# Optimization experiments

Hardware: AMD Instinct MI355X
Metric: run time of the kernel (lower is better)

## Reference

```python
import jax, jax.numpy as jnp
import numpy as np

NUM_HEADS = 16

def setup_inputs() -> dict:
    key = jax.random.key(0)
    k1, k2, k3, k4 = jax.random.split(key, 4)
    B, S, E = 4, 2048, 1024
    return {
        "q": jax.random.normal(k1, (B, S, E), dtype=jnp.float32),
        "k": jax.random.normal(k2, (B, S, E), dtype=jnp.float32),
        "v": jax.random.normal(k3, (B, S, E), dtype=jnp.float32),
        "w_out": jax.random.normal(k4, (E, E), dtype=jnp.float32) * (E ** -0.5),
        "b_out": jnp.zeros((E,), dtype=jnp.float32),
    }

def reference(q, k, v, w_out, b_out):
    B, S, E = q.shape
    H = NUM_HEADS
    D = E // H
    scale = D ** -0.5
    # split heads: [B, S, E] -> [B, H, S, D]
    def split(x):
        return x.reshape(B, S, H, D).transpose(0, 2, 1, 3)
    qh, kh, vh = split(q), split(k), split(v)
    scores = jnp.einsum('bhqd,bhkd->bhqk', qh, kh) * scale  # [B,H,S,S]
    weights = jax.nn.softmax(scores, axis=-1)
    # dropout is identity in eval mode
    out = jnp.einsum('bhqk,bhkd->bhqd', weights, vh)
    out = out.transpose(0, 2, 1, 3).reshape(B, S, E)  # merge heads
    return out @ w_out.T + b_out
```

## Files before the change

kernel.cpp:

```cpp
#include <hip/hip_runtime.h>
#include <cstdint>
#include <cstddef>

typedef __attribute__((ext_vector_type(8))) short bf16x8;
typedef __attribute__((ext_vector_type(4))) float f32x4;
typedef __attribute__((ext_vector_type(16))) float f32x16;

#define MFMA16(a, b, c) __builtin_amdgcn_mfma_f32_16x16x32_bf16((a), (b), (c), 0, 0, 0)
#define MFMA32(a, b, c) __builtin_amdgcn_mfma_f32_32x32x16_bf16((a), (b), (c), 0, 0, 0)

constexpr int Bz = 4, S = 2048, E = 1024, H = 16, Dh = 64;
constexpr size_t BSE = (size_t)Bz * S * E;
constexpr int LDP = 72;
constexpr int VLD = 136;

__device__ __forceinline__ unsigned short f2bf(float f) {
    uint32_t u = __builtin_bit_cast(uint32_t, f);
    u += 0x7FFFu + ((u >> 16) & 1u);
    return (unsigned short)(u >> 16);
}

__device__ __forceinline__ float exp2_fast(float x) {
#if __has_builtin(__builtin_amdgcn_exp2f)
    return __builtin_amdgcn_exp2f(x);
#else
    return exp2f(x);
#endif
}

__device__ __forceinline__ uint32_t pack_bf16(float a, float b) {
    uint32_t ua = __builtin_bit_cast(uint32_t, a) + 0x8000u;
    uint32_t ub = __builtin_bit_cast(uint32_t, b) + 0x8000u;
#if __has_builtin(__builtin_amdgcn_perm)
    return __builtin_amdgcn_perm(ub, ua, 0x07060302u);
#else
    return (ua >> 16) | (ub & 0xFFFF0000u);
#endif
}

__global__ __launch_bounds__(256) void convert_kernel(const float* __restrict__ in,
                                                      unsigned short* __restrict__ out,
                                                      int n4, float scale) {
    int i = blockIdx.x * blockDim.x + threadIdx.x;
    if (i < n4) {
        float4 f = ((const float4*)in)[i];
        ushort4 u;
        u.x = f2bf(f.x * scale);
        u.y = f2bf(f.y * scale);
        u.z = f2bf(f.z * scale);
        u.w = f2bf(f.w * scale);
        ((ushort4*)out)[i] = u;
    }
}

__global__ __launch_bounds__(256) void transpose_v_kernel(const float* __restrict__ v,
                                                          unsigned short* __restrict__ vt) {
    __shared__ unsigned short tile[64][65];
    const int b = blockIdx.z, h = blockIdx.y, s0 = blockIdx.x * 64;
    const int r = threadIdx.x >> 2, cb = (threadIdx.x & 3) * 16;

    const float* src = v + ((size_t)(b * S + s0 + r) * E + h * Dh + cb);
#pragma unroll
    for (int j = 0; j < 16; j += 4) {
        float4 f = *(const float4*)(src + j);
        tile[cb + j + 0][r] = f2bf(f.x);
        tile[cb + j + 1][r] = f2bf(f.y);
        tile[cb + j + 2][r] = f2bf(f.z);
        tile[cb + j + 3][r] = f2bf(f.w);
    }
    __syncthreads();
    const int dv = threadIdx.x >> 2, seg = (threadIdx.x & 3) * 16;
    unsigned short* dst = vt + (((size_t)(b * H + h) * Dh + dv) * S + s0 + seg);
    uint4 w0, w1;
    const unsigned short* trow = &tile[dv][seg];
    w0 = *(const uint4*)(trow);
    w1 = *(const uint4*)(trow + 8);
    *(uint4*)(dst) = w0;
    *(uint4*)(dst + 8) = w1;
}

__global__ __launch_bounds__(256, 4) void attn_kernel(const float* __restrict__ q,
                                                      const unsigned short* __restrict__ kb,
                                                      const unsigned short* __restrict__ vt,
                                                      unsigned short* __restrict__ attn) {
    __shared__ unsigned short smem[128 * LDP + 64 * VLD];
    unsigned short* Ks = smem;
    unsigned short* Vts = smem + 128 * LDP;

    const int b = blockIdx.z, h = blockIdx.y, qblk = blockIdx.x;
    const int tid = threadIdx.x;
    const int wave = tid >> 6, lane = tid & 63;
    const int l32 = lane & 31, half = lane >> 5;

    const int q0 = qblk * 128 + wave * 32;
    const float scl = 0.125f * 1.44269504088896f;

    bf16x8 qreg[4];
    {
        const float* qsrc = q + ((size_t)(b * S + q0 + l32)) * E + h * Dh + half * 8;
#pragma unroll
        for (int t = 0; t < 4; ++t) {
            float4 f0 = *(const float4*)(qsrc + 16 * t);
            float4 f1 = *(const float4*)(qsrc + 16 * t + 4);
            bf16x8 r;
            r[0] = (short)f2bf(f0.x * scl); r[1] = (short)f2bf(f0.y * scl);
            r[2] = (short)f2bf(f0.z * scl); r[3] = (short)f2bf(f0.w * scl);
            r[4] = (short)f2bf(f1.x * scl); r[5] = (short)f2bf(f1.y * scl);
            r[6] = (short)f2bf(f1.z * scl); r[7] = (short)f2bf(f1.w * scl);
            qreg[t] = r;
        }
    }

    f32x16 oacc[2];
#pragma unroll
    for (int mt = 0; mt < 2; ++mt)
#pragma unroll
        for (int r = 0; r < 16; ++r) oacc[mt][r] = 0.f;
    float lp0 = 0.f, lp1 = 0.f, lp2 = 0.f, lp3 = 0.f;

    const int krow = tid >> 1, kseg = (tid & 1) * 32;
    const int vrow = tid >> 2, vseg = (tid & 3) * 32;
    const unsigned short* kbase = kb + ((size_t)(b * S) * E + h * Dh);
    const unsigned short* vbase = vt + ((size_t)((b * H + h) * Dh + vrow) * S);

    for (int kt = 0; kt < S / 128; ++kt) {
        __syncthreads();
        {
            const uint4* ksrc = (const uint4*)(kbase + (size_t)(kt * 128 + krow) * E + kseg);
            uint4* kdst = (uint4*)(Ks + krow * LDP + kseg);
#pragma unroll
            for (int u = 0; u < 4; ++u) kdst[u] = ksrc[u];
            const uint4* vsrc = (const uint4*)(vbase + kt * 128 + vseg);
            uint4* vdst = (uint4*)(Vts + vrow * VLD + vseg);
#pragma unroll
            for (int u = 0; u < 4; ++u) vdst[u] = vsrc[u];
        }
        __syncthreads();

#pragma unroll
        for (int kh = 0; kh < 2; ++kh) {
            f32x16 st[2];
#pragma unroll
            for (int mt = 0; mt < 2; ++mt) {
#pragma unroll
                for (int r = 0; r < 16; ++r) st[mt][r] = 0.f;
#pragma unroll
                for (int t = 0; t < 4; ++t) {
                    bf16x8 a = *(const bf16x8*)(Ks + (kh * 64 + mt * 32 + l32) * LDP +
                                                t * 16 + half * 8);
                    st[mt] = MFMA32(a, qreg[t], st[mt]);
                }
            }

            uint32_t pkd[2][4][2];
#pragma unroll
            for (int mt = 0; mt < 2; ++mt)
#pragma unroll
                for (int g = 0; g < 4; ++g) {
                    float p0 = exp2_fast(st[mt][4 * g + 0]);
                    float p1 = exp2_fast(st[mt][4 * g + 1]);
                    float p2 = exp2_fast(st[mt][4 * g + 2]);
                    float p3 = exp2_fast(st[mt][4 * g + 3]);
                    lp0 += p0; lp1 += p1; lp2 += p2; lp3 += p3;
                    pkd[mt][g][0] = pack_bf16(p0, p1);
                    pkd[mt][g][1] = pack_bf16(p2, p3);
                }

#pragma unroll
            for (int c = 0; c < 4; ++c) {
                const int ms = c >> 1;
                const int g0 = 2 * (c & 1);
                uint32_t a0 = pkd[ms][g0][0], a1 = pkd[ms][g0][1];
                uint32_t b0 = pkd[ms][g0 + 1][0], b1 = pkd[ms][g0 + 1][1];
                uint32_t snd0 = half ? a0 : b0;
                uint32_t snd1 = half ? a1 : b1;
                uint32_t r0 = (uint32_t)__shfl_xor((int)snd0, 32);
                uint32_t r1 = (uint32_t)__shfl_xor((int)snd1, 32);
                int4 bi;
                bi.x = (int)(half ? r0 : a0);
                bi.y = (int)(half ? r1 : a1);
                bi.z = (int)(half ? b0 : r0);
                bi.w = (int)(half ? b1 : r1);
                bf16x8 bfrag = __builtin_bit_cast(bf16x8, bi);
#pragma unroll
                for (int mt = 0; mt < 2; ++mt) {
                    bf16x8 a = *(const bf16x8*)(Vts + (mt * 32 + l32) * VLD +
                                                kh * 64 + c * 16 + half * 8);
                    oacc[mt] = MFMA32(a, bfrag, oacc[mt]);
                }
            }
        }
    }

    __syncthreads();
    float l_part = (lp0 + lp1) + (lp2 + lp3);
    float l = l_part + (float)__shfl_xor(l_part, 32);
    float inv = 1.0f / l;

    unsigned short* ob = smem + wave * (32 * LDP);
#pragma unroll
    for (int mt = 0; mt < 2; ++mt)
#pragma unroll
        for (int g = 0; g < 4; ++g) {
            int dv0 = 8 * g + 4 * half + 32 * mt;
            uint2 w2;
            w2.x = pack_bf16(oacc[mt][4 * g + 0] * inv, oacc[mt][4 * g + 1] * inv);
            w2.y = pack_bf16(oacc[mt][4 * g + 2] * inv, oacc[mt][4 * g + 3] * inv);
            *(uint2*)(ob + l32 * LDP + dv0) = w2;
        }
    __syncthreads();
    {
        int row = lane >> 1;
        int cg0 = (lane & 1) * 4;
        unsigned short* gdst = attn + ((size_t)(b * S + q0 + row)) * E + h * Dh;
#pragma unroll
        for (int j = 0; j < 4; ++j) {
            bf16x8 v8 = *(const bf16x8*)(ob + row * LDP + (cg0 + j) * 8);
            *(bf16x8*)(gdst + (cg0 + j) * 8) = v8;
        }
    }
}

constexpr int PLD = 40;
__global__ __launch_bounds__(256) void proj_kernel(const unsigned short* __restrict__ A,
                                                   const unsigned short* __restrict__ W,
                                                   const float* __restrict__ bias,
                                                   float* __restrict__ C) {
    __shared__ unsigned short As[128 * PLD];
    __shared__ unsigned short Bs[128 * PLD];
    const int tid = threadIdx.x;
    const int wave = tid >> 6, lane = tid & 63, quad = lane >> 4, l16 = lane & 15;
    const int wm = wave >> 1, wn = wave & 1;
    const int m0 = blockIdx.x * 128, n0 = blockIdx.y * 128;

    f32x4 acc[4][4];
    f32x4 zero = {0.f, 0.f, 0.f, 0.f};
#pragma unroll
    for (int mi = 0; mi < 4; ++mi)
#pragma unroll
        for (int ni = 0; ni < 4; ++ni) acc[mi][ni] = zero;

    const int srow = tid >> 1, scb = (tid & 1) * 16;

    for (int k0 = 0; k0 < 1024; k0 += 32) {
        __syncthreads();
        {
            const uint4* asrc = (const uint4*)(A + (size_t)(m0 + srow) * 1024 + k0 + scb);
            uint4* adst = (uint4*)(As + srow * PLD + scb);
            adst[0] = asrc[0];
            adst[1] = asrc[1];
            const uint4* bsrc = (const uint4*)(W + (size_t)(n0 + srow) * 1024 + k0 + scb);
            uint4* bdst = (uint4*)(Bs + srow * PLD + scb);
            bdst[0] = bsrc[0];
            bdst[1] = bsrc[1];
        }
        __syncthreads();

        bf16x8 af[4], bfr[4];
#pragma unroll
        for (int mi = 0; mi < 4; ++mi)
            af[mi] = *(const bf16x8*)(As + (wm * 64 + mi * 16 + l16) * PLD + quad * 8);
#pragma unroll
        for (int ni = 0; ni < 4; ++ni)
            bfr[ni] = *(const bf16x8*)(Bs + (wn * 64 + ni * 16 + l16) * PLD + quad * 8);
#pragma unroll
        for (int mi = 0; mi < 4; ++mi)
#pragma unroll
            for (int ni = 0; ni < 4; ++ni)
                acc[mi][ni] = MFMA16(af[mi], bfr[ni], acc[mi][ni]);
    }

    float bb[4];
#pragma unroll
    for (int ni = 0; ni < 4; ++ni) bb[ni] = bias[n0 + wn * 64 + ni * 16 + l16];
#pragma unroll
    for (int mi = 0; mi < 4; ++mi) {
        const int row = m0 + wm * 64 + mi * 16 + quad * 4;
#pragma unroll
        for (int ni = 0; ni < 4; ++ni) {
            const int col = n0 + wn * 64 + ni * 16 + l16;
#pragma unroll
            for (int r = 0; r < 4; ++r)
                C[(size_t)(row + r) * 1024 + col] = acc[mi][ni][r] + bb[ni];
        }
    }
}

extern "C" void kernel_launch(void* const* d_in, const int* in_sizes, int n_in,
                              void* d_out, int out_size, void* d_ws, size_t ws_size,
                              hipStream_t stream) {
    const float* q = (const float*)d_in[0];
    const float* k = (const float*)d_in[1];
    const float* v = (const float*)d_in[2];
    const float* w = (const float*)d_in[3];
    const float* bias = (const float*)d_in[4];
    float* out = (float*)d_out;

    unsigned short* ws = (unsigned short*)d_ws;
    unsigned short* kb = ws;
    unsigned short* vt = kb + BSE;
    unsigned short* wb = vt + BSE;
    unsigned short* attnb = wb + (size_t)E * E;

    {
        int n4 = (int)(BSE / 4);
        convert_kernel<<<dim3((n4 + 255) / 256), dim3(256), 0, stream>>>(k, kb, n4, 1.0f);
        int nw4 = (int)((size_t)E * E / 4);
        convert_kernel<<<dim3((nw4 + 255) / 256), dim3(256), 0, stream>>>(w, wb, nw4, 1.0f);
    }
    transpose_v_kernel<<<dim3(S / 64, H, Bz), dim3(256), 0, stream>>>(v, vt);
    attn_kernel<<<dim3(S / 128, H, Bz), dim3(256), 0, stream>>>(q, kb, vt, attnb);
    proj_kernel<<<dim3((Bz * S) / 128, E / 128), dim3(256), 0, stream>>>(attnb, wb, bias, out);
}
```

Baseline: 287.9 us.

## Fuse K/V prep, prefetch tiles in registers, remap blocks, use 32x32 MFMA projection

```diff
diff --git a/kernel.cpp b/kernel.cpp
--- a/kernel.cpp
+++ b/kernel.cpp
@@ -6,7 +6,6 @@
 typedef __attribute__((ext_vector_type(4))) float f32x4;
 typedef __attribute__((ext_vector_type(16))) float f32x16;
 
-#define MFMA16(a, b, c) __builtin_amdgcn_mfma_f32_16x16x32_bf16((a), (b), (c), 0, 0, 0)
 #define MFMA32(a, b, c) __builtin_amdgcn_mfma_f32_32x32x16_bf16((a), (b), (c), 0, 0, 0)
 
 constexpr int Bz = 4, S = 2048, E = 1024, H = 16, Dh = 64;
@@ -38,45 +37,43 @@
 #endif
 }
 
-__global__ __launch_bounds__(256) void convert_kernel(const float* __restrict__ in,
-                                                      unsigned short* __restrict__ out,
-                                                      int n4, float scale) {
-    int i = blockIdx.x * blockDim.x + threadIdx.x;
-    if (i < n4) {
-        float4 f = ((const float4*)in)[i];
-        ushort4 u;
-        u.x = f2bf(f.x * scale);
-        u.y = f2bf(f.y * scale);
-        u.z = f2bf(f.z * scale);
-        u.w = f2bf(f.w * scale);
-        ((ushort4*)out)[i] = u;
-    }
-}
-
-__global__ __launch_bounds__(256) void transpose_v_kernel(const float* __restrict__ v,
-                                                          unsigned short* __restrict__ vt) {
+__global__ __launch_bounds__(256) void prep_kv(const float* __restrict__ k,
+                                               const float* __restrict__ v,
+                                               unsigned short* __restrict__ kb,
+                                               unsigned short* __restrict__ vt) {
     __shared__ unsigned short tile[64][65];
     const int b = blockIdx.z, h = blockIdx.y, s0 = blockIdx.x * 64;
     const int r = threadIdx.x >> 2, cb = (threadIdx.x & 3) * 16;
-
-    const float* src = v + ((size_t)(b * S + s0 + r) * E + h * Dh + cb);
-#pragma unroll
-    for (int j = 0; j < 16; j += 4) {
-        float4 f = *(const float4*)(src + j);
-        tile[cb + j + 0][r] = f2bf(f.x);
-        tile[cb + j + 1][r] = f2bf(f.y);
-        tile[cb + j + 2][r] = f2bf(f.z);
-        tile[cb + j + 3][r] = f2bf(f.w);
+    const size_t off = (size_t)(b * S + s0 + r) * E + h * Dh + cb;
+
+    {
+        const float* src = k + off;
+        uint32_t o[8];
+#pragma unroll
+        for (int j = 0; j < 8; ++j) {
+            float2 f = *(const float2*)(src + 2 * j);
+            o[j] = pack_bf16(f.x, f.y);
+        }
+        unsigned short* dst = kb + off;
+        *(uint4*)(dst) = *(const uint4*)(o);
+        *(uint4*)(dst + 8) = *(const uint4*)(o + 4);
+    }
+    {
+        const float* src = v + off;
+#pragma unroll
+        for (int j = 0; j < 16; j += 4) {
+            float4 f = *(const float4*)(src + j);
+            tile[cb + j + 0][r] = f2bf(f.x);
+            tile[cb + j + 1][r] = f2bf(f.y);
+            tile[cb + j + 2][r] = f2bf(f.z);
+            tile[cb + j + 3][r] = f2bf(f.w);
+        }
     }
     __syncthreads();
     const int dv = threadIdx.x >> 2, seg = (threadIdx.x & 3) * 16;
     unsigned short* dst = vt + (((size_t)(b * H + h) * Dh + dv) * S + s0 + seg);
-    uint4 w0, w1;
-    const unsigned short* trow = &tile[dv][seg];
-    w0 = *(const uint4*)(trow);
-    w1 = *(const uint4*)(trow + 8);
-    *(uint4*)(dst) = w0;
-    *(uint4*)(dst + 8) = w1;
+    *(uint4*)(dst) = *(const uint4*)(&tile[dv][seg]);
+    *(uint4*)(dst + 8) = *(const uint4*)(&tile[dv][seg] + 8);
 }
 
 __global__ __launch_bounds__(256, 4) void attn_kernel(const float* __restrict__ q,
@@ -87,7 +84,11 @@
     unsigned short* Ks = smem;
     unsigned short* Vts = smem + 128 * LDP;
 
-    const int b = blockIdx.z, h = blockIdx.y, qblk = blockIdx.x;
+    const int wid = blockIdx.x + 16 * (blockIdx.y + 16 * blockIdx.z);
+    const int c_ = wid & 7, j_ = wid >> 3;
+    const int bh = c_ * 8 + (j_ >> 4), qblk = j_ & 15;
+    const int b = bh >> 4, h = bh & 15;
+
     const int tid = threadIdx.x;
     const int wave = tid >> 6, lane = tid & 63;
     const int l32 = lane & 31, half = lane >> 5;
@@ -123,19 +124,36 @@
     const unsigned short* kbase = kb + ((size_t)(b * S) * E + h * Dh);
     const unsigned short* vbase = vt + ((size_t)((b * H + h) * Dh + vrow) * S);
 
+    uint4 kpre[4], vpre[4];
+    {
+        const uint4* ksrc = (const uint4*)(kbase + (size_t)krow * E + kseg);
+#pragma unroll
+        for (int u = 0; u < 4; ++u) kpre[u] = ksrc[u];
+        const uint4* vsrc = (const uint4*)(vbase + vseg);
+#pragma unroll
+        for (int u = 0; u < 4; ++u) vpre[u] = vsrc[u];
+    }
+
     for (int kt = 0; kt < S / 128; ++kt) {
         __syncthreads();
         {
-            const uint4* ksrc = (const uint4*)(kbase + (size_t)(kt * 128 + krow) * E + kseg);
             uint4* kdst = (uint4*)(Ks + krow * LDP + kseg);
 #pragma unroll
-            for (int u = 0; u < 4; ++u) kdst[u] = ksrc[u];
-            const uint4* vsrc = (const uint4*)(vbase + kt * 128 + vseg);
+            for (int u = 0; u < 4; ++u) kdst[u] = kpre[u];
             uint4* vdst = (uint4*)(Vts + vrow * VLD + vseg);
 #pragma unroll
-            for (int u = 0; u < 4; ++u) vdst[u] = vsrc[u];
+            for (int u = 0; u < 4; ++u) vdst[u] = vpre[u];
         }
         __syncthreads();
+
+        if (kt + 1 < S / 128) {
+            const uint4* ksrc = (const uint4*)(kbase + (size_t)((kt + 1) * 128 + krow) * E + kseg);
+#pragma unroll
+            for (int u = 0; u < 4; ++u) kpre[u] = ksrc[u];
+            const uint4* vsrc = (const uint4*)(vbase + (kt + 1) * 128 + vseg);
+#pragma unroll
+            for (int u = 0; u < 4; ++u) vpre[u] = vsrc[u];
+        }
 
 #pragma unroll
         for (int kh = 0; kh < 2; ++kh) {
@@ -222,66 +240,98 @@
 }
 
 constexpr int PLD = 40;
-__global__ __launch_bounds__(256) void proj_kernel(const unsigned short* __restrict__ A,
-                                                   const unsigned short* __restrict__ W,
-                                                   const float* __restrict__ bias,
-                                                   float* __restrict__ C) {
+__global__ __launch_bounds__(256, 4) void proj_kernel(const unsigned short* __restrict__ A,
+                                                      const float* __restrict__ W,
+                                                      const float* __restrict__ bias,
+                                                      float* __restrict__ C) {
     __shared__ unsigned short As[128 * PLD];
     __shared__ unsigned short Bs[128 * PLD];
     const int tid = threadIdx.x;
-    const int wave = tid >> 6, lane = tid & 63, quad = lane >> 4, l16 = lane & 15;
+    const int wave = tid >> 6, lane = tid & 63;
+    const int l32 = lane & 31, half = lane >> 5;
     const int wm = wave >> 1, wn = wave & 1;
     const int m0 = blockIdx.x * 128, n0 = blockIdx.y * 128;
 
-    f32x4 acc[4][4];
-    f32x4 zero = {0.f, 0.f, 0.f, 0.f};
-#pragma unroll
-    for (int mi = 0; mi < 4; ++mi)
-#pragma unroll
-        for (int ni = 0; ni < 4; ++ni) acc[mi][ni] = zero;
+    f32x16 acc[2][2];
+#pragma unroll
+    for (int mi = 0; mi < 2; ++mi)
+#pragma unroll
+        for (int ni = 0; ni < 2; ++ni)
+#pragma unroll
+            for (int r = 0; r < 16; ++r) acc[mi][ni][r] = 0.f;
 
     const int srow = tid >> 1, scb = (tid & 1) * 16;
+
+    uint4 apre[2];
+    float4 wpre[4];
+    {
+        const uint4* asrc = (const uint4*)(A + (size_t)(m0 + srow) * 1024 + scb);
+        apre[0] = asrc[0];
+        apre[1] = asrc[1];
+        const float4* wsrc = (const float4*)(W + (size_t)(n0 + srow) * 1024 + scb);
+#pragma unroll
+        for (int u = 0; u < 4; ++u) wpre[u] = wsrc[u];
+    }
 
     for (int k0 = 0; k0 < 1024; k0 += 32) {
         __syncthreads();
         {
-            const uint4* asrc = (const uint4*)(A + (size_t)(m0 + srow) * 1024 + k0 + scb);
             uint4* adst = (uint4*)(As + srow * PLD + scb);
-            adst[0] = asrc[0];
-            adst[1] = asrc[1];
-            const uint4* bsrc = (const uint4*)(W + (size_t)(n0 + srow) * 1024 + k0 + scb);
+            adst[0] = apre[0];
+            adst[1] = apre[1];
+            uint32_t pw[8];
+            const float* wf = (const float*)wpre;
+#pragma unroll
+            for (int j = 0; j < 8; ++j) pw[j] = pack_bf16(wf[2 * j], wf[2 * j + 1]);
             uint4* bdst = (uint4*)(Bs + srow * PLD + scb);
-            bdst[0] = bsrc[0];
-            bdst[1] = bsrc[1];
+            bdst[0] = *(const uint4*)(pw);
+            bdst[1] = *(const uint4*)(pw + 4);
         }
         __syncthreads();
 
-        bf16x8 af[4], bfr[4];
-#pragma unroll
-        for (int mi = 0; mi < 4; ++mi)
-            af[mi] = *(const bf16x8*)(As + (wm * 64 + mi * 16 + l16) * PLD + quad * 8);
-#pragma unroll
-        for (int ni = 0; ni < 4; ++ni)
-            bfr[ni] = *(const bf16x8*)(Bs + (wn * 64 + ni * 16 + l16) * PLD + quad * 8);
-#pragma unroll
-        for (int mi = 0; mi < 4; ++mi)
-#pragma unroll
-            for (int ni = 0; ni < 4; ++ni)
-                acc[mi][ni] = MFMA16(af[mi], bfr[ni], acc[mi][ni]);
-    }
-
-    float bb[4];
-#pragma unroll
-    for (int ni = 0; ni < 4; ++ni) bb[ni] = bias[n0 + wn * 64 + ni * 16 + l16];
-#pragma unroll
-    for (int mi = 0; mi < 4; ++mi) {
-        const int row = m0 + wm * 64 + mi * 16 + quad * 4;
-#pragma unroll
-        for (int ni = 0; ni < 4; ++ni) {
-            const int col = n0 + wn * 64 + ni * 16 + l16;
-#pragma unroll
-            for (int r = 0; r < 4; ++r)
-                C[(size_t)(row + r) * 1024 + col] = acc[mi][ni][r] + bb[ni];
+        if (k0 + 32 < 1024) {
+            const uint4* asrc = (const uint4*)(A + (size_t)(m0 + srow) * 1024 + k0 + 32 + scb);
+            apre[0] = asrc[0];
+            apre[1] = asrc[1];
+            const float4* wsrc = (const float4*)(W + (size_t)(n0 + srow) * 1024 + k0 + 32 + scb);
+#pragma unroll
+            for (int u = 0; u < 4; ++u) wpre[u] = wsrc[u];
+        }
+
+        bf16x8 af[2][2], bfr[2][2];
+#pragma unroll
+        for (int ks = 0; ks < 2; ++ks) {
+#pragma unroll
+            for (int mi = 0; mi < 2; ++mi)
+                af[ks][mi] = *(const bf16x8*)(As + (wm * 64 + mi * 32 + l32) * PLD +
+                                              ks * 16 + half * 8);
+#pragma unroll
+            for (int ni = 0; ni < 2; ++ni)
+                bfr[ks][ni] = *(const bf16x8*)(Bs + (wn * 64 + ni * 32 + l32) * PLD +
+                                               ks * 16 + half * 8);
+        }
+#pragma unroll
+        for (int ks = 0; ks < 2; ++ks)
+#pragma unroll
+            for (int mi = 0; mi < 2; ++mi)
+#pragma unroll
+                for (int ni = 0; ni < 2; ++ni)
+                    acc[mi][ni] = MFMA32(af[ks][mi], bfr[ks][ni], acc[mi][ni]);
+    }
+
+    float bb[2];
+#pragma unroll
+    for (int ni = 0; ni < 2; ++ni) bb[ni] = bias[n0 + wn * 64 + ni * 32 + l32];
+#pragma unroll
+    for (int mi = 0; mi < 2; ++mi) {
+#pragma unroll
+        for (int ni = 0; ni < 2; ++ni) {
+            const int col = n0 + wn * 64 + ni * 32 + l32;
+#pragma unroll
+            for (int r = 0; r < 16; ++r) {
+                int row = m0 + wm * 64 + mi * 32 + (r & 3) + 8 * (r >> 2) + 4 * half;
+                C[(size_t)row * 1024 + col] = acc[mi][ni][r] + bb[ni];
+            }
         }
     }
 }
@@ -299,16 +349,9 @@
     unsigned short* ws = (unsigned short*)d_ws;
     unsigned short* kb = ws;
     unsigned short* vt = kb + BSE;
-    unsigned short* wb = vt + BSE;
-    unsigned short* attnb = wb + (size_t)E * E;
-
-    {
-        int n4 = (int)(BSE / 4);
-        convert_kernel<<<dim3((n4 + 255) / 256), dim3(256), 0, stream>>>(k, kb, n4, 1.0f);
-        int nw4 = (int)((size_t)E * E / 4);
-        convert_kernel<<<dim3((nw4 + 255) / 256), dim3(256), 0, stream>>>(w, wb, nw4, 1.0f);
-    }
-    transpose_v_kernel<<<dim3(S / 64, H, Bz), dim3(256), 0, stream>>>(v, vt);
+    unsigned short* attnb = vt + BSE;
+
+    prep_kv<<<dim3(S / 64, H, Bz), dim3(256), 0, stream>>>(k, v, kb, vt);
     attn_kernel<<<dim3(S / 128, H, Bz), dim3(256), 0, stream>>>(q, kb, vt, attnb);
-    proj_kernel<<<dim3((Bz * S) / 128, E / 128), dim3(256), 0, stream>>>(attnb, wb, bias, out);
-}
+    proj_kernel<<<dim3((Bz * S) / 128, E / 128), dim3(256), 0, stream>>>(attnb, w, bias, out);
+}
```

Measured after the change: 410.4 us. +42.5%, slower.

## Double-buffer K/V via direct-to-LDS loads, enlarge query tile, fuse K/V prep

Applied to the files above, without the earlier changes.

```diff
diff --git a/kernel.cpp b/kernel.cpp
--- a/kernel.cpp
+++ b/kernel.cpp
@@ -11,8 +11,6 @@
 
 constexpr int Bz = 4, S = 2048, E = 1024, H = 16, Dh = 64;
 constexpr size_t BSE = (size_t)Bz * S * E;
-constexpr int LDP = 72;
-constexpr int VLD = 136;
 
 __device__ __forceinline__ unsigned short f2bf(float f) {
     uint32_t u = __builtin_bit_cast(uint32_t, f);
@@ -38,66 +36,87 @@
 #endif
 }
 
+__device__ __forceinline__ void gload16(const unsigned short* g, unsigned short* l) {
+    __builtin_amdgcn_global_load_lds((const __attribute__((address_space(1))) void*)g,
+                                     (__attribute__((address_space(3))) void*)l, 16, 0, 0);
+}
+
 __global__ __launch_bounds__(256) void convert_kernel(const float* __restrict__ in,
                                                       unsigned short* __restrict__ out,
-                                                      int n4, float scale) {
+                                                      int n4) {
     int i = blockIdx.x * blockDim.x + threadIdx.x;
     if (i < n4) {
         float4 f = ((const float4*)in)[i];
-        ushort4 u;
-        u.x = f2bf(f.x * scale);
-        u.y = f2bf(f.y * scale);
-        u.z = f2bf(f.z * scale);
-        u.w = f2bf(f.w * scale);
-        ((ushort4*)out)[i] = u;
-    }
-}
-
-__global__ __launch_bounds__(256) void transpose_v_kernel(const float* __restrict__ v,
-                                                          unsigned short* __restrict__ vt) {
+        uint2 u;
+        u.x = pack_bf16(f.x, f.y);
+        u.y = pack_bf16(f.z, f.w);
+        ((uint2*)out)[i] = u;
+    }
+}
+
+__global__ __launch_bounds__(256) void prep_kv(const float* __restrict__ k,
+                                               const float* __restrict__ v,
+                                               unsigned short* __restrict__ kb,
+                                               unsigned short* __restrict__ vt) {
     __shared__ unsigned short tile[64][65];
     const int b = blockIdx.z, h = blockIdx.y, s0 = blockIdx.x * 64;
     const int r = threadIdx.x >> 2, cb = (threadIdx.x & 3) * 16;
-
-    const float* src = v + ((size_t)(b * S + s0 + r) * E + h * Dh + cb);
-#pragma unroll
-    for (int j = 0; j < 16; j += 4) {
-        float4 f = *(const float4*)(src + j);
-        tile[cb + j + 0][r] = f2bf(f.x);
-        tile[cb + j + 1][r] = f2bf(f.y);
-        tile[cb + j + 2][r] = f2bf(f.z);
-        tile[cb + j + 3][r] = f2bf(f.w);
+    const size_t off = (size_t)(b * S + s0 + r) * E + h * Dh + cb;
+
+    {
+        const float* src = k + off;
+        uint32_t o[8];
+#pragma unroll
+        for (int j = 0; j < 8; ++j) {
+            float2 f = *(const float2*)(src + 2 * j);
+            o[j] = pack_bf16(f.x, f.y);
+        }
+        unsigned short* dst = kb + off;
+        *(uint4*)(dst) = *(const uint4*)(o);
+        *(uint4*)(dst + 8) = *(const uint4*)(o + 4);
+    }
+    {
+        const float* src = v + off;
+#pragma unroll
+        for (int j = 0; j < 16; j += 4) {
+            float4 f = *(const float4*)(src + j);
+            tile[cb + j + 0][r] = f2bf(f.x);
+            tile[cb + j + 1][r] = f2bf(f.y);
+            tile[cb + j + 2][r] = f2bf(f.z);
+            tile[cb + j + 3][r] = f2bf(f.w);
+        }
     }
     __syncthreads();
     const int dv = threadIdx.x >> 2, seg = (threadIdx.x & 3) * 16;
     unsigned short* dst = vt + (((size_t)(b * H + h) * Dh + dv) * S + s0 + seg);
-    uint4 w0, w1;
-    const unsigned short* trow = &tile[dv][seg];
-    w0 = *(const uint4*)(trow);
-    w1 = *(const uint4*)(trow + 8);
-    *(uint4*)(dst) = w0;
-    *(uint4*)(dst + 8) = w1;
-}
-
-__global__ __launch_bounds__(256, 4) void attn_kernel(const float* __restrict__ q,
+    *(uint4*)(dst) = *(const uint4*)(&tile[dv][seg]);
+    *(uint4*)(dst + 8) = *(const uint4*)(&tile[dv][seg] + 8);
+}
+
+constexpr int GSTR = 528;
+__global__ __launch_bounds__(256, 2) void attn_kernel(const float* __restrict__ q,
                                                       const unsigned short* __restrict__ kb,
                                                       const unsigned short* __restrict__ vt,
                                                       unsigned short* __restrict__ attn) {
-    __shared__ unsigned short smem[128 * LDP + 64 * VLD];
-    unsigned short* Ks = smem;
-    unsigned short* Vts = smem + 128 * LDP;
-
-    const int b = blockIdx.z, h = blockIdx.y, qblk = blockIdx.x;
+    __shared__ unsigned short smem[18432];
+
+    const int wid = blockIdx.x + 8 * (blockIdx.y + 16 * blockIdx.z);
+    const int c_ = wid & 7, j_ = wid >> 3;
+    const int bh = c_ * 8 + (j_ >> 3), qblk = j_ & 7;
+    const int b = bh >> 4, h = bh & 15;
+
     const int tid = threadIdx.x;
     const int wave = tid >> 6, lane = tid & 63;
     const int l32 = lane & 31, half = lane >> 5;
-
-    const int q0 = qblk * 128 + wave * 32;
+    const int x7 = l32 & 7, y4 = l32 >> 3;
+
+    const int q0 = qblk * 256 + wave * 64;
     const float scl = 0.125f * 1.44269504088896f;
 
-    bf16x8 qreg[4];
-    {
-        const float* qsrc = q + ((size_t)(b * S + q0 + l32)) * E + h * Dh + half * 8;
+    bf16x8 qreg[2][4];
+#pragma unroll
+    for (int qh = 0; qh < 2; ++qh) {
+        const float* qsrc = q + ((size_t)(b * S + q0 + qh * 32 + l32)) * E + h * Dh + half * 8;
 #pragma unroll
         for (int t = 0; t < 4; ++t) {
             float4 f0 = *(const float4*)(qsrc + 16 * t);
@@ -107,71 +126,102 @@
             r[2] = (short)f2bf(f0.z * scl); r[3] = (short)f2bf(f0.w * scl);
             r[4] = (short)f2bf(f1.x * scl); r[5] = (short)f2bf(f1.y * scl);
             r[6] = (short)f2bf(f1.z * scl); r[7] = (short)f2bf(f1.w * scl);
-            qreg[t] = r;
-        }
-    }
-
-    f32x16 oacc[2];
-#pragma unroll
-    for (int mt = 0; mt < 2; ++mt)
-#pragma unroll
-        for (int r = 0; r < 16; ++r) oacc[mt][r] = 0.f;
-    float lp0 = 0.f, lp1 = 0.f, lp2 = 0.f, lp3 = 0.f;
-
-    const int krow = tid >> 1, kseg = (tid & 1) * 32;
-    const int vrow = tid >> 2, vseg = (tid & 3) * 32;
-    const unsigned short* kbase = kb + ((size_t)(b * S) * E + h * Dh);
-    const unsigned short* vbase = vt + ((size_t)((b * H + h) * Dh + vrow) * S);
-
-    for (int kt = 0; kt < S / 128; ++kt) {
+            qreg[qh][t] = r;
+        }
+    }
+
+    f32x16 fzero;
+#pragma unroll
+    for (int r = 0; r < 16; ++r) fzero[r] = 0.f;
+    f32x16 oacc[2][2];
+#pragma unroll
+    for (int qh = 0; qh < 2; ++qh)
+#pragma unroll
+        for (int mt = 0; mt < 2; ++mt) oacc[qh][mt] = fzero;
+    float lsum[2] = {0.f, 0.f};
+
+    const int row8 = lane >> 3;
+    const int sg = (lane & 7) ^ row8;
+    const unsigned short* kbase = kb + ((size_t)(b * S)) * E + h * Dh;
+    const unsigned short* vtb = vt + ((size_t)(b * H + h) * Dh) * S;
+
+    auto stage = [&](int kt, int bsel) {
+        unsigned short* ksb = smem + bsel * 8448;
+        unsigned short* vsb = ksb + 4224;
+#pragma unroll
+        for (int u = 0; u < 2; ++u) {
+            const int gi = wave * 2 + u;
+            gload16(kbase + (size_t)(kt * 64 + gi * 8 + row8) * E + sg * 8, ksb + gi * GSTR);
+            gload16(vtb + (size_t)(gi * 8 + row8) * S + kt * 64 + sg * 8, vsb + gi * GSTR);
+        }
+    };
+
+    int roff[2];
+#pragma unroll
+    for (int mt = 0; mt < 2; ++mt) roff[mt] = (mt * 4 + y4) * GSTR + x7 * 64;
+
+    constexpr int NT = S / 64;
+    stage(0, 0);
+
+    for (int kt = 0; kt < NT; ++kt) {
+        const int cur = kt & 1;
         __syncthreads();
-        {
-            const uint4* ksrc = (const uint4*)(kbase + (size_t)(kt * 128 + krow) * E + kseg);
-            uint4* kdst = (uint4*)(Ks + krow * LDP + kseg);
-#pragma unroll
-            for (int u = 0; u < 4; ++u) kdst[u] = ksrc[u];
-            const uint4* vsrc = (const uint4*)(vbase + kt * 128 + vseg);
-            uint4* vdst = (uint4*)(Vts + vrow * VLD + vseg);
-#pragma unroll
-            for (int u = 0; u < 4; ++u) vdst[u] = vsrc[u];
-        }
-        __syncthreads();
-
-#pragma unroll
-        for (int kh = 0; kh < 2; ++kh) {
-            f32x16 st[2];
+        if (kt + 1 < NT) stage(kt + 1, cur ^ 1);
+        const unsigned short* ksb = smem + cur * 8448;
+        const unsigned short* vsb = ksb + 4224;
+
+        bf16x8 kfrag[2][4];
+#pragma unroll
+        for (int mt = 0; mt < 2; ++mt)
+#pragma unroll
+            for (int t = 0; t < 4; ++t)
+                kfrag[mt][t] = *(const bf16x8*)(ksb + roff[mt] + (((t * 2 + half) ^ x7) * 8));
+
+        f32x16 st[2][2];
+#pragma unroll
+        for (int qh = 0; qh < 2; ++qh)
 #pragma unroll
             for (int mt = 0; mt < 2; ++mt) {
-#pragma unroll
-                for (int r = 0; r < 16; ++r) st[mt][r] = 0.f;
-#pragma unroll
-                for (int t = 0; t < 4; ++t) {
-                    bf16x8 a = *(const bf16x8*)(Ks + (kh * 64 + mt * 32 + l32) * LDP +
-                                                t * 16 + half * 8);
-                    st[mt] = MFMA32(a, qreg[t], st[mt]);
+                st[qh][mt] = MFMA32(kfrag[mt][0], qreg[qh][0], fzero);
+#pragma unroll
+                for (int t = 1; t < 4; ++t)
+                    st[qh][mt] = MFMA32(kfrag[mt][t], qreg[qh][t], st[qh][mt]);
+            }
+
+        uint32_t pkd[2][2][4][2];
+#pragma unroll
+        for (int qh = 0; qh < 2; ++qh) {
+            float ls = 0.f;
+#pragma unroll
+            for (int mt = 0; mt < 2; ++mt)
+#pragma unroll
+                for (int g = 0; g < 4; ++g) {
+                    float p0 = exp2_fast(st[qh][mt][4 * g + 0]);
+                    float p1 = exp2_fast(st[qh][mt][4 * g + 1]);
+                    float p2 = exp2_fast(st[qh][mt][4 * g + 2]);
+                    float p3 = exp2_fast(st[qh][mt][4 * g + 3]);
+                    ls += (p0 + p1) + (p2 + p3);
+                    pkd[qh][mt][g][0] = pack_bf16(p0, p1);
+                    pkd[qh][mt][g][1] = pack_bf16(p2, p3);
                 }
-            }
-
-            uint32_t pkd[2][4][2];
-#pragma unroll
-            for (int mt = 0; mt < 2; ++mt)
-#pragma unroll
-                for (int g = 0; g < 4; ++g) {
-                    float p0 = exp2_fast(st[mt][4 * g + 0]);
-                    float p1 = exp2_fast(st[mt][4 * g + 1]);
-                    float p2 = exp2_fast(st[mt][4 * g + 2]);
-                    float p3 = exp2_fast(st[mt][4 * g + 3]);
-                    lp0 += p0; lp1 += p1; lp2 += p2; lp3 += p3;
-                    pkd[mt][g][0] = pack_bf16(p0, p1);
-                    pkd[mt][g][1] = pack_bf16(p2, p3);
-                }
-
+            lsum[qh] += ls;
+        }
+
+        bf16x8 vfrag[2][4];
+#pragma unroll
+        for (int mt = 0; mt < 2; ++mt)
+#pragma unroll
+            for (int c = 0; c < 4; ++c)
+                vfrag[mt][c] = *(const bf16x8*)(vsb + roff[mt] + (((c * 2 + half) ^ x7) * 8));
+
+#pragma unroll
+        for (int qh = 0; qh < 2; ++qh)
 #pragma unroll
             for (int c = 0; c < 4; ++c) {
                 const int ms = c >> 1;
                 const int g0 = 2 * (c & 1);
-                uint32_t a0 = pkd[ms][g0][0], a1 = pkd[ms][g0][1];
-                uint32_t b0 = pkd[ms][g0 + 1][0], b1 = pkd[ms][g0 + 1][1];
+                uint32_t a0 = pkd[qh][ms][g0][0], a1 = pkd[qh][ms][g0][1];
+                uint32_t b0 = pkd[qh][ms][g0 + 1][0], b1 = pkd[qh][ms][g0 + 1][1];
                 uint32_t snd0 = half ? a0 : b0;
                 uint32_t snd1 = half ? a1 : b1;
                 uint32_t r0 = (uint32_t)__shfl_xor((int)snd0, 32);
@@ -183,40 +233,44 @@
                 bi.w = (int)(half ? b1 : r1);
                 bf16x8 bfrag = __builtin_bit_cast(bf16x8, bi);
 #pragma unroll
-                for (int mt = 0; mt < 2; ++mt) {
-                    bf16x8 a = *(const bf16x8*)(Vts + (mt * 32 + l32) * VLD +
-                                                kh * 64 + c * 16 + half * 8);
-                    oacc[mt] = MFMA32(a, bfrag, oacc[mt]);
-                }
+                for (int mt = 0; mt < 2; ++mt)
+                    oacc[qh][mt] = MFMA32(vfrag[mt][c], bfrag, oacc[qh][mt]);
             }
-        }
     }
 
     __syncthreads();
-    float l_part = (lp0 + lp1) + (lp2 + lp3);
-    float l = l_part + (float)__shfl_xor(l_part, 32);
-    float inv = 1.0f / l;
-
-    unsigned short* ob = smem + wave * (32 * LDP);
-#pragma unroll
-    for (int mt = 0; mt < 2; ++mt)
-#pragma unroll
-        for (int g = 0; g < 4; ++g) {
-            int dv0 = 8 * g + 4 * half + 32 * mt;
-            uint2 w2;
-            w2.x = pack_bf16(oacc[mt][4 * g + 0] * inv, oacc[mt][4 * g + 1] * inv);
-            w2.y = pack_bf16(oacc[mt][4 * g + 2] * inv, oacc[mt][4 * g + 3] * inv);
-            *(uint2*)(ob + l32 * LDP + dv0) = w2;
-        }
+    float inv[2];
+#pragma unroll
+    for (int qh = 0; qh < 2; ++qh) {
+        float l = lsum[qh] + (float)__shfl_xor(lsum[qh], 32);
+        inv[qh] = 1.0f / l;
+    }
+
+    unsigned short* ob = smem + wave * (64 * 72);
+#pragma unroll
+    for (int qh = 0; qh < 2; ++qh)
+#pragma unroll
+        for (int mt = 0; mt < 2; ++mt)
+#pragma unroll
+            for (int g = 0; g < 4; ++g) {
+                int dv0 = 8 * g + 4 * half + 32 * mt;
+                uint2 w2;
+                w2.x = pack_bf16(oacc[qh][mt][4 * g + 0] * inv[qh],
+                                 oacc[qh][mt][4 * g + 1] * inv[qh]);
+                w2.y = pack_bf16(oacc[qh][mt][4 * g + 2] * inv[qh],
+                                 oacc[qh][mt][4 * g + 3] * inv[qh]);
+                *(uint2*)(ob + (qh * 32 + l32) * 72 + dv0) = w2;
+            }
     __syncthreads();
-    {
-        int row = lane >> 1;
-        int cg0 = (lane & 1) * 4;
-        unsigned short* gdst = attn + ((size_t)(b * S + q0 + row)) * E + h * Dh;
+#pragma unroll
+    for (int it = 0; it < 2; ++it) {
+        int row = it * 32 + (lane >> 1);
+        int seg = (lane & 1) * 32;
+        unsigned short* gdst = attn + ((size_t)(b * S + q0 + row)) * E + h * Dh + seg;
 #pragma unroll
         for (int j = 0; j < 4; ++j) {
-            bf16x8 v8 = *(const bf16x8*)(ob + row * LDP + (cg0 + j) * 8);
-            *(bf16x8*)(gdst + (cg0 + j) * 8) = v8;
+            bf16x8 v8 = *(const bf16x8*)(ob + row * 72 + seg + j * 8);
+            *(bf16x8*)(gdst + j * 8) = v8;
         }
     }
 }
@@ -299,16 +353,14 @@
     unsigned short* ws = (unsigned short*)d_ws;
     unsigned short* kb = ws;
     unsigned short* vt = kb + BSE;
-    unsigned short* wb = vt + BSE;
-    unsigned short* attnb = wb + (size_t)E * E;
-
+    unsigned short* attnb = vt + BSE;
+    unsigned short* wb = attnb + BSE;
+
+    prep_kv<<<dim3(S / 64, H, Bz), dim3(256), 0, stream>>>(k, v, kb, vt);
     {
-        int n4 = (int)(BSE / 4);
-        convert_kernel<<<dim3((n4 + 255) / 256), dim3(256), 0, stream>>>(k, kb, n4, 1.0f);
         int nw4 = (int)((size_t)E * E / 4);
-        convert_kernel<<<dim3((nw4 + 255) / 256), dim3(256), 0, stream>>>(w, wb, nw4, 1.0f);
-    }
-    transpose_v_kernel<<<dim3(S / 64, H, Bz), dim3(256), 0, stream>>>(v, vt);
-    attn_kernel<<<dim3(S / 128, H, Bz), dim3(256), 0, stream>>>(q, kb, vt, attnb);
+        convert_kernel<<<dim3((nw4 + 255) / 256), dim3(256), 0, stream>>>(w, wb, nw4);
+    }
+    attn_kernel<<<dim3(S / 256, H, Bz), dim3(256), 0, stream>>>(q, kb, vt, attnb);
     proj_kernel<<<dim3((Bz * S) / 128, E / 128), dim3(256), 0, stream>>>(attnb, wb, bias, out);
 }
```

Result: faster. 255.5 us (-11.3%).
